# Performance work log

Measured on AMD Instinct MI355X. Metric: run time of the kernel, lower is better.

## Reference

```python
import jax, jax.numpy as jnp
import numpy as np

IN_FEATURES = 4096
OUT_FEATURES = 4096
SPARSE_RATIO = 0.1
NNZ = int(IN_FEATURES * OUT_FEATURES * SPARSE_RATIO)  # 1677721
N_COLS = 4096  # x is (out_features, N); bias broadcast requires N == out_features


def setup_inputs() -> dict:
    key = jax.random.key(0)
    k_x, k_r, k_c, k_v, k_b = jax.random.split(key, 5)
    x = jax.random.normal(k_x, (OUT_FEATURES, N_COLS), dtype=jnp.float32)
    rows = jax.random.randint(k_r, (NNZ,), 0, IN_FEATURES, dtype=jnp.int32)
    cols = jax.random.randint(k_c, (NNZ,), 0, OUT_FEATURES, dtype=jnp.int32)
    vals = jax.random.normal(k_v, (NNZ,), dtype=jnp.float32)
    bias = jax.random.normal(k_b, (OUT_FEATURES,), dtype=jnp.float32)
    return {"x": x, "rows": rows, "cols": cols, "vals": vals, "bias": bias}


def reference(x, rows, cols, vals, bias):
    # Scatter the COO weight into its dense form once (duplicate coords
    # accumulate, matching sparse COO coalescing semantics), then do a
    # dense GEMM: y = W @ x + bias. Same math as torch.sparse.mm.
    W = jnp.zeros((IN_FEATURES, OUT_FEATURES), dtype=x.dtype).at[rows, cols].add(vals)
    return W @ x + bias  # (in_features, N) + (out_features,) broadcast on last axis
```

## Files before the change

kernel.cpp:

```cpp
#include <hip/hip_runtime.h>
#include <hip/hip_bf16.h>
#include <stdint.h>

#define MDIM 4096
#define NDIM 4096
#define KDIM 4096

typedef float f32x4 __attribute__((ext_vector_type(4)));
typedef __bf16 bf16x8 __attribute__((ext_vector_type(8)));
typedef short s16x8 __attribute__((ext_vector_type(8)));


__device__ __forceinline__ unsigned short f2bf(float x) {
  union { float f; unsigned u; } v; v.f = x;
  return (unsigned short)((v.u + 0x7fffu + ((v.u >> 16) & 1u)) >> 16);
}

__device__ __forceinline__ void scat_one(unsigned short* __restrict__ Wpk,
                                         int m, int k, float val) {
  unsigned short bits = f2bf(val);
  size_t chunk = ((((size_t)(m >> 7) * 128 + (k >> 5)) * 8 + ((m >> 4) & 7)) * 64) +
                 (((k >> 3) & 3) * 16 + (m & 15));
  size_t idx = chunk * 8 + (k & 7);
  unsigned data = ((unsigned)bits) << ((unsigned)(idx & 1) * 16u);
  unsigned short* p = &Wpk[idx & ~(size_t)1];
  asm volatile("global_atomic_pk_add_bf16 %0, %1, off" :: "v"(p), "v"(data) : "memory");
}

#define ZBLOCKS 8192
__global__ __launch_bounds__(256) void prep_zero_pack(float* __restrict__ Wz,
                                                      const float* __restrict__ x,
                                                      short* __restrict__ Xpk) {
  int b = blockIdx.x, tid = threadIdx.x;
  if (b < ZBLOCKS) {
    ((f32x4*)Wz)[(size_t)b * 256 + tid] = f32x4{0.f, 0.f, 0.f, 0.f};
  } else {
    __shared__ float tile[32 * 65];
    int pb = b - ZBLOCKS;
    int n0 = (pb & 63) * 64, k0 = (pb >> 6) * 32;
#pragma unroll
    for (int r = 0; r < 8; r++) {
      int elem = r * 256 + tid;
      int kk = elem >> 6, nn = elem & 63;
      tile[kk * 65 + nn] = x[(size_t)(k0 + kk) * NDIM + n0 + nn];
    }
    __syncthreads();
    int region = tid >> 6, lane = tid & 63;
    int kh = lane >> 4, nl = region * 16 + (lane & 15);
    s16x8 v;
#pragma unroll
    for (int j = 0; j < 8; j++) v[j] = (short)f2bf(tile[(kh * 8 + j) * 65 + nl]);
    int f = ((n0 & 127) >> 4) + region;
    size_t chunk = (((size_t)(n0 >> 7) * 128 + (k0 >> 5)) * 8 + f) * 64 + lane;
    *(s16x8*)&Xpk[chunk * 8] = v;
  }
}

__global__ __launch_bounds__(256) void scatter_kernel(const int* __restrict__ rows,
                                                      const int* __restrict__ cols,
                                                      const float* __restrict__ vals, int nnz,
                                                      unsigned short* __restrict__ Wpk) {
  int i0 = (blockIdx.x * 256 + threadIdx.x) * 4;
  if (i0 >= nnz) return;
  if (i0 + 3 < nnz) {
    int4 r4 = *(const int4*)&rows[i0];
    int4 c4 = *(const int4*)&cols[i0];
    float4 v4 = *(const float4*)&vals[i0];
    scat_one(Wpk, r4.x, c4.x, v4.x);
    scat_one(Wpk, r4.y, c4.y, v4.y);
    scat_one(Wpk, r4.z, c4.z, v4.z);
    scat_one(Wpk, r4.w, c4.w, v4.w);
  } else {
    for (int u = 0; u < 4 && i0 + u < nnz; u++)
      scat_one(Wpk, rows[i0 + u], cols[i0 + u], vals[i0 + u]);
  }
}


#define GLOAD16(gp, lp)                                              \
  __builtin_amdgcn_global_load_lds(                                  \
      (const __attribute__((address_space(1))) void*)(gp),           \
      (__attribute__((address_space(3))) void*)(lp), 16, 0, 0)

__global__ __launch_bounds__(512, 2) void gemm_kernel(const short* __restrict__ A,
                                                      const short* __restrict__ Bt,
                                                      const float* __restrict__ bias,
                                                      float* __restrict__ C) {
  __shared__ __align__(16) short sA[4][8192];
  __shared__ __align__(16) short sB[4][8192];

  int tid = threadIdx.x, lane = tid & 63, w = tid >> 6;
  int wr = w >> 2, wc = w & 3;
  int m16 = lane & 15, quad = lane >> 4;
  int by = blockIdx.y, bx = blockIdx.x;

  f32x4 acc[8][4];
#pragma unroll
  for (int i = 0; i < 8; i++)
#pragma unroll
    for (int j = 0; j < 4; j++) acc[i][j] = f32x4{0.f, 0.f, 0.f, 0.f};

  const short* aSrc[2];
  const short* bSrc[2];
  int ldsOff[2];
#pragma unroll
  for (int s = 0; s < 2; s++) {
    aSrc[s] = A + ((size_t)(2 * by + s) * 128 * 8 + w) * 512 + lane * 8;
    bSrc[s] = Bt + ((size_t)(2 * bx + s) * 128 * 8 + w) * 512 + lane * 8;
    ldsOff[s] = (s * 8 + w) * 512 + lane * 8;
  }

#pragma unroll
  for (int t = 0; t < 3; t++) {
    GLOAD16(aSrc[0] + (size_t)t * 4096, &sA[t][ldsOff[0]]);
    GLOAD16(aSrc[1] + (size_t)t * 4096, &sA[t][ldsOff[1]]);
    GLOAD16(bSrc[0] + (size_t)t * 4096, &sB[t][ldsOff[0]]);
    GLOAD16(bSrc[1] + (size_t)t * 4096, &sB[t][ldsOff[1]]);
  }
  __builtin_amdgcn_s_waitcnt(0x0F78);
  __builtin_amdgcn_s_barrier();

  for (int t = 0; t < 128; t++) {
    int buf = t & 3;
    int nbuf = (t + 3) & 3;
    size_t tn = (size_t)((t + 3) & 127) * 4096;

    const short* pA = &sA[buf][0];
    const short* pB = &sB[buf][0];
    bf16x8 a[4], b[4], a2[4];

#pragma unroll
    for (int mi = 0; mi < 4; mi++)
      a[mi] = *(const bf16x8*)&pA[(wr * 8 + mi) * 512 + lane * 8];
#pragma unroll
    for (int nj = 0; nj < 4; nj++)
      b[nj] = *(const bf16x8*)&pB[((wc >> 1) * 8 + (wc & 1) * 4 + nj) * 512 + lane * 8];
#pragma unroll
    for (int mi = 0; mi < 4; mi++)
      a2[mi] = *(const bf16x8*)&pA[(wr * 8 + 4 + mi) * 512 + lane * 8];

    GLOAD16(aSrc[0] + tn, &sA[nbuf][ldsOff[0]]);
    GLOAD16(aSrc[1] + tn, &sA[nbuf][ldsOff[1]]);
    __builtin_amdgcn_s_barrier();

    __builtin_amdgcn_s_setprio(1);
#pragma unroll
    for (int mi = 0; mi < 4; mi++)
#pragma unroll
      for (int nj = 0; nj < 4; nj++)
        acc[mi][nj] = __builtin_amdgcn_mfma_f32_16x16x32_bf16(a[mi], b[nj], acc[mi][nj], 0, 0, 0);
    __builtin_amdgcn_s_setprio(0);

    GLOAD16(bSrc[0] + tn, &sB[nbuf][ldsOff[0]]);
    GLOAD16(bSrc[1] + tn, &sB[nbuf][ldsOff[1]]);

    __builtin_amdgcn_s_setprio(1);
#pragma unroll
    for (int mi = 0; mi < 4; mi++)
#pragma unroll
      for (int nj = 0; nj < 4; nj++)
        acc[4 + mi][nj] = __builtin_amdgcn_mfma_f32_16x16x32_bf16(a2[mi], b[nj], acc[4 + mi][nj], 0, 0, 0);
    __builtin_amdgcn_s_setprio(0);

    __builtin_amdgcn_s_waitcnt(0x0F78);
    __builtin_amdgcn_s_barrier();
  }
  __builtin_amdgcn_s_waitcnt(0x0F70);

#pragma unroll
  for (int nj = 0; nj < 4; nj++) {
    int col = bx * 256 + wc * 64 + nj * 16 + m16;
    float bv = bias[col];
#pragma unroll
    for (int mi = 0; mi < 8; mi++) {
      int row0 = by * 256 + wr * 128 + mi * 16 + quad * 4;
      f32x4 v = acc[mi][nj];
#pragma unroll
      for (int r = 0; r < 4; r++) C[(size_t)(row0 + r) * NDIM + col] = v[r] + bv;
    }
  }
}

extern "C" void kernel_launch(void* const* d_in, const int* in_sizes, int n_in,
                              void* d_out, int out_size, void* d_ws, size_t ws_size,
                              hipStream_t stream) {
  const float* x = (const float*)d_in[0];
  const int* rows = (const int*)d_in[1];
  const int* cols = (const int*)d_in[2];
  const float* vals = (const float*)d_in[3];
  const float* bias = (const float*)d_in[4];
  int nnz = in_sizes[1];
  float* y = (float*)d_out;

  char* ws = (char*)d_ws;
  unsigned short* Wpk = (unsigned short*)ws;
  short* Xpk = (short*)(ws + (32u << 20));

  int scBlocks = (nnz + 1023) / 1024;
  int pxBlocks = (NDIM / 64) * (KDIM / 32);

  prep_zero_pack<<<ZBLOCKS + pxBlocks, 256, 0, stream>>>((float*)Wpk, x, Xpk);
  scatter_kernel<<<scBlocks, 256, 0, stream>>>(rows, cols, vals, nnz, Wpk);
  gemm_kernel<<<dim3(NDIM / 256, MDIM / 256), 512, 0, stream>>>((const short*)Wpk, Xpk, bias, y);
}
```

Before: 337.1 us.

## Load GEMM B fragments directly from global into registers, bypassing LDS

The B operand tile no longer goes through LDS. Each wave now reads its four B fragments straight from global memory into registers, double-buffered one k-step ahead in a ping-pong unrolled loop, while A keeps its 4-stage LDS pipeline. This removes the B LDS writes and reads, halves shared-memory use and drops one barrier per iteration. In exchange, waves in different rows now issue duplicate B loads, and global load latency is covered by only one iteration of register prefetch.

Result: no change. 342.7 us (+1.7%).

```diff
diff --git a/kernel.cpp b/kernel.cpp
--- a/kernel.cpp
+++ b/kernel.cpp
@@ -87,7 +87,6 @@
                                                       const float* __restrict__ bias,
                                                       float* __restrict__ C) {
   __shared__ __align__(16) short sA[4][8192];
-  __shared__ __align__(16) short sB[4][8192];
 
   int tid = threadIdx.x, lane = tid & 63, w = tid >> 6;
   int wr = w >> 2, wc = w & 3;
@@ -101,70 +100,54 @@
     for (int j = 0; j < 4; j++) acc[i][j] = f32x4{0.f, 0.f, 0.f, 0.f};
 
   const short* aSrc[2];
-  const short* bSrc[2];
   int ldsOff[2];
 #pragma unroll
   for (int s = 0; s < 2; s++) {
     aSrc[s] = A + ((size_t)(2 * by + s) * 128 * 8 + w) * 512 + lane * 8;
-    bSrc[s] = Bt + ((size_t)(2 * bx + s) * 128 * 8 + w) * 512 + lane * 8;
     ldsOff[s] = (s * 8 + w) * 512 + lane * 8;
   }
+  const short* bBase = Bt + ((size_t)((2 * bx + (wc >> 1)) * 1024 + (wc & 1) * 4)) * 512 + lane * 8;
 
 #pragma unroll
   for (int t = 0; t < 3; t++) {
     GLOAD16(aSrc[0] + (size_t)t * 4096, &sA[t][ldsOff[0]]);
     GLOAD16(aSrc[1] + (size_t)t * 4096, &sA[t][ldsOff[1]]);
-    GLOAD16(bSrc[0] + (size_t)t * 4096, &sB[t][ldsOff[0]]);
-    GLOAD16(bSrc[1] + (size_t)t * 4096, &sB[t][ldsOff[1]]);
   }
-  __builtin_amdgcn_s_waitcnt(0x0F78);
+  bf16x8 bC[4], bN[4];
+#pragma unroll
+  for (int nj = 0; nj < 4; nj++)
+    bC[nj] = *(const bf16x8*)(bBase + (size_t)nj * 512);
+  __builtin_amdgcn_s_waitcnt(0x0F76);
   __builtin_amdgcn_s_barrier();
 
-  for (int t = 0; t < 128; t++) {
-    int buf = t & 3;
-    int nbuf = (t + 3) & 3;
-    size_t tn = (size_t)((t + 3) & 127) * 4096;
+#define HALF_ITER(T, BUSE, BLOAD)                                                    \
+  {                                                                                  \
+    int t_ = (T);                                                                    \
+    const short* pA = &sA[t_ & 3][0];                                                \
+    bf16x8 a[8];                                                                     \
+    _Pragma("unroll") for (int mi = 0; mi < 8; mi++)                                 \
+        a[mi] = *(const bf16x8*)&pA[(wr * 8 + mi) * 512 + lane * 8];                 \
+    int tl_ = (t_ + 1) & 127;         \
+    _Pragma("unroll") for (int nj = 0; nj < 4; nj++)                                 \
+        BLOAD[nj] = *(const bf16x8*)(bBase + ((size_t)tl_ * 8 + nj) * 512);          \
+    size_t tn_ = (size_t)((t_ + 3) & 127) * 4096;                                    \
+    GLOAD16(aSrc[0] + tn_, &sA[(t_ + 3) & 3][ldsOff[0]]);                            \
+    GLOAD16(aSrc[1] + tn_, &sA[(t_ + 3) & 3][ldsOff[1]]);                            \
+    __builtin_amdgcn_s_setprio(1);                                                   \
+    _Pragma("unroll") for (int mi = 0; mi < 8; mi++)                                 \
+        _Pragma("unroll") for (int nj = 0; nj < 4; nj++)                             \
+            acc[mi][nj] =                                                            \
+        __builtin_amdgcn_mfma_f32_16x16x32_bf16(a[mi], BUSE[nj], acc[mi][nj], 0, 0, 0); \
+    __builtin_amdgcn_s_setprio(0);                                                   \
+    __builtin_amdgcn_s_waitcnt(0x0F76);         \
+    __builtin_amdgcn_s_barrier();                                                    \
+  }
 
-    const short* pA = &sA[buf][0];
-    const short* pB = &sB[buf][0];
-    bf16x8 a[4], b[4], a2[4];
-
-#pragma unroll
-    for (int mi = 0; mi < 4; mi++)
-      a[mi] = *(const bf16x8*)&pA[(wr * 8 + mi) * 512 + lane * 8];
-#pragma unroll
-    for (int nj = 0; nj < 4; nj++)
-      b[nj] = *(const bf16x8*)&pB[((wc >> 1) * 8 + (wc & 1) * 4 + nj) * 512 + lane * 8];
-#pragma unroll
-    for (int mi = 0; mi < 4; mi++)
-      a2[mi] = *(const bf16x8*)&pA[(wr * 8 + 4 + mi) * 512 + lane * 8];
-
-    GLOAD16(aSrc[0] + tn, &sA[nbuf][ldsOff[0]]);
-    GLOAD16(aSrc[1] + tn, &sA[nbuf][ldsOff[1]]);
-    __builtin_amdgcn_s_barrier();
-
-    __builtin_amdgcn_s_setprio(1);
-#pragma unroll
-    for (int mi = 0; mi < 4; mi++)
-#pragma unroll
-      for (int nj = 0; nj < 4; nj++)
-        acc[mi][nj] = __builtin_amdgcn_mfma_f32_16x16x32_bf16(a[mi], b[nj], acc[mi][nj], 0, 0, 0);
-    __builtin_amdgcn_s_setprio(0);
-
-    GLOAD16(bSrc[0] + tn, &sB[nbuf][ldsOff[0]]);
-    GLOAD16(bSrc[1] + tn, &sB[nbuf][ldsOff[1]]);
-
-    __builtin_amdgcn_s_setprio(1);
-#pragma unroll
-    for (int mi = 0; mi < 4; mi++)
-#pragma unroll
-      for (int nj = 0; nj < 4; nj++)
-        acc[4 + mi][nj] = __builtin_amdgcn_mfma_f32_16x16x32_bf16(a2[mi], b[nj], acc[4 + mi][nj], 0, 0, 0);
-    __builtin_amdgcn_s_setprio(0);
-
-    __builtin_amdgcn_s_waitcnt(0x0F78);
-    __builtin_amdgcn_s_barrier();
+  for (int u = 0; u < 64; u++) {
+    HALF_ITER(2 * u, bC, bN)
+    HALF_ITER(2 * u + 1, bN, bC)
   }
+#undef HALF_ITER
   __builtin_amdgcn_s_waitcnt(0x0F70);
 
 #pragma unroll
```
